# Performance work log

Measured on AMD Instinct MI355X. Metric: run time of the kernel, lower is better.

The kernel has to match this reference:

```python
import jax, jax.numpy as jnp
import numpy as np

D = 8        # num_decoders
N = 65536    # num_entries
LAT = 64     # latent_dim
HID = 128    # hidden_dim_dec
FEAT = 16    # feature_dim


def setup_inputs() -> dict:
    key = jax.random.key(0)
    ks = jax.random.split(key, 6)
    return {
        "weight": jax.random.normal(ks[0], (N, LAT), jnp.float32) * 2.0,
        "alpha_param": jax.random.normal(ks[1], (D, N), jnp.float32),  # alpha_std=1.0
        "div": jnp.ones((LAT,), jnp.float32),
        "scale0": jax.random.normal(ks[2], (D, LAT, HID), jnp.float32),  # ldec_std=1.0 normal init
        "shift0": jnp.zeros((D, 1, HID), jnp.float32),
        "scale1": jax.random.normal(ks[3], (D, HID, HID), jnp.float32),
        "shift1": jnp.zeros((D, 1, HID), jnp.float32),
        "scale2": jax.random.normal(ks[4], (D, HID, FEAT), jnp.float32),
        "shift2": jnp.zeros((D, 1, FEAT), jnp.float32),
    }


def _st_round(x):
    # StraightThrough: round in forward, identity gradient
    return x + jax.lax.stop_gradient(jnp.round(x) - x)


def _layer(x, alpha, scale, shift):
    # x: [N, I], alpha: [D, N], scale: [D, I, O], shift: [D, 1, O]
    out = jnp.einsum('ni,dio->dno', x, scale)           # per-decoder GEMMs [D,N,O]
    mix = jnp.einsum('dno,dn->no', out, alpha)          # alpha-weighted combine
    # second alpha-weighted sum over (mix + per-decoder shift), as in the torch code
    return jnp.einsum('dno,dn->no', mix[None, :, :] + shift, alpha)


def reference(weight, alpha_param, div, scale0, shift0, scale1, shift1, scale2, shift2):
    temperature = 1.0
    a = jax.nn.softmax(alpha_param / temperature, axis=0)       # [D, N]
    idx = jnp.argmax(a, axis=0)                                 # [N]
    onehot = jax.nn.one_hot(idx, a.shape[0], dtype=a.dtype).T   # [D, N]
    alpha = a + jax.lax.stop_gradient(onehot - a)               # straight-through one-hot

    x = _st_round(weight) / div                                 # [N, LAT]
    x = jax.nn.relu(_layer(x, alpha, scale0, shift0))           # [N, HID]
    x = jax.nn.relu(_layer(x, alpha, scale1, shift1))           # [N, HID]
    out = _layer(x, alpha, scale2, shift2)                      # [N, FEAT], final_activation='none'
    return out
```

## Files before the change

### kernel.cpp

```cpp
#include <hip/hip_runtime.h>

#define NN 65536
#define DD 8
#define LATD 64
#define HIDD 128
#define FEATD 16
#define BPD 96
#define SXS 72
#define SHS 136

typedef __attribute__((ext_vector_type(8))) short short8;
typedef __attribute__((ext_vector_type(4))) float f32x4;

static __device__ __forceinline__ unsigned short f2bf(float f) {
  union { float f; unsigned u; } v; v.f = f;
  unsigned r = v.u + 0x7FFFu + ((v.u >> 16) & 1u);
  return (unsigned short)(r >> 16);
}

__global__ __launch_bounds__(256) void k_bucket(const float* __restrict__ ap,
                                                int* __restrict__ cursor,
                                                unsigned short* __restrict__ perm) {
  __shared__ int bc[DD];
  __shared__ int bbase[DD];
  int t = threadIdx.x;
  if (t < DD) bc[t] = 0;
  __syncthreads();
  int n = blockIdx.x * 256 + t;
  float best = ap[n];
  int bd = 0;
#pragma unroll
  for (int d = 1; d < DD; ++d) {
    float v = ap[d * NN + n];
    if (v > best) { best = v; bd = d; }
  }
  int lr = atomicAdd(&bc[bd], 1);
  __syncthreads();
  if (t < DD) bbase[t] = atomicAdd(&cursor[t], bc[t]);
  __syncthreads();
  perm[bd * NN + bbase[bd] + lr] = (unsigned short)n;
}

__global__ __launch_bounds__(256, 3) void k_mlp(
    const float* __restrict__ weight, const float* __restrict__ divv,
    const float* __restrict__ s0, const float* __restrict__ sh0,
    const float* __restrict__ s1, const float* __restrict__ sh1,
    const float* __restrict__ s2, const float* __restrict__ sh2,
    const int* __restrict__ cursor, const unsigned short* __restrict__ perm,
    float* __restrict__ out) {
  __shared__ unsigned short sX[64 * SXS];
  __shared__ unsigned short sH1[64 * SHS];
  __shared__ unsigned short sH2[64 * SHS];
  __shared__ unsigned short sP[64];

  int d = blockIdx.x / BPD, bslot = blockIdx.x % BPD;
  int cnt = cursor[d];
  int t = threadIdx.x;
  int w = t >> 6, l = t & 63;
  int lrow = l & 15, kgrp = l >> 4;

  short8 b0[2][2];
  short8 b1[2][4];
  short8 b2[4];
  float sh0v[2], sh1v[2];
  const float* S0 = s0 + d * LATD * HIDD;
  const float* S1 = s1 + d * HIDD * HIDD;
  const float* S2 = s2 + d * HIDD * FEATD;
#pragma unroll
  for (int cb = 0; cb < 2; ++cb) {
    int n = (2 * w + cb) * 16 + lrow;
#pragma unroll
    for (int ks = 0; ks < 2; ++ks) {
      short8 v;
#pragma unroll
      for (int j = 0; j < 8; ++j)
        v[j] = (short)f2bf(S0[(ks * 32 + kgrp * 8 + j) * HIDD + n]);
      b0[cb][ks] = v;
    }
#pragma unroll
    for (int ks = 0; ks < 4; ++ks) {
      short8 v;
#pragma unroll
      for (int j = 0; j < 8; ++j)
        v[j] = (short)f2bf(S1[(ks * 32 + kgrp * 8 + j) * HIDD + n]);
      b1[cb][ks] = v;
    }
    sh0v[cb] = sh0[d * HIDD + n];
    sh1v[cb] = sh1[d * HIDD + n];
  }
#pragma unroll
  for (int ks = 0; ks < 4; ++ks) {
    short8 v;
#pragma unroll
    for (int j = 0; j < 8; ++j)
      v[j] = (short)f2bf(S2[(ks * 32 + kgrp * 8 + j) * FEATD + lrow]);
    b2[ks] = v;
  }
  float sh2v = sh2[d * FEATD + lrow];

  for (int tile = bslot; tile * 64 < cnt; tile += BPD) {
    int base = tile * 64;

    {
      int r = t >> 2, c = t & 3;
      int gp = base + r;
      unsigned short pe = 0;
      short8 lo = {0, 0, 0, 0, 0, 0, 0, 0}, hi = {0, 0, 0, 0, 0, 0, 0, 0};
      if (gp < cnt) {
        pe = perm[d * NN + gp];
        const float* wr = weight + (int)pe * LATD + c * 16;
        const float* dv = divv + c * 16;
#pragma unroll
        for (int q = 0; q < 2; ++q) {
          float4 f = *(const float4*)(wr + q * 4);
          float4 g = *(const float4*)(dv + q * 4);
          lo[q * 4 + 0] = (short)f2bf(rintf(f.x) / g.x);
          lo[q * 4 + 1] = (short)f2bf(rintf(f.y) / g.y);
          lo[q * 4 + 2] = (short)f2bf(rintf(f.z) / g.z);
          lo[q * 4 + 3] = (short)f2bf(rintf(f.w) / g.w);
        }
#pragma unroll
        for (int q = 0; q < 2; ++q) {
          float4 f = *(const float4*)(wr + 8 + q * 4);
          float4 g = *(const float4*)(dv + 8 + q * 4);
          hi[q * 4 + 0] = (short)f2bf(rintf(f.x) / g.x);
          hi[q * 4 + 1] = (short)f2bf(rintf(f.y) / g.y);
          hi[q * 4 + 2] = (short)f2bf(rintf(f.z) / g.z);
          hi[q * 4 + 3] = (short)f2bf(rintf(f.w) / g.w);
        }
      }
      if (c == 0) sP[r] = pe;
      *(short8*)&sX[r * SXS + c * 16] = lo;
      *(short8*)&sX[r * SXS + c * 16 + 8] = hi;
    }
    __syncthreads();

    int prow[4];
#pragma unroll
    for (int rr = 0; rr < 4; ++rr) prow[rr] = (int)sP[w * 16 + kgrp * 4 + rr];

#pragma unroll
    for (int rg = 0; rg < 4; ++rg) {
      short8 a0 = *(short8*)&sX[(rg * 16 + lrow) * SXS + kgrp * 8];
      short8 a1 = *(short8*)&sX[(rg * 16 + lrow) * SXS + 32 + kgrp * 8];
#pragma unroll
      for (int cb = 0; cb < 2; ++cb) {
        f32x4 acc = {sh0v[cb], sh0v[cb], sh0v[cb], sh0v[cb]};
        acc = __builtin_amdgcn_mfma_f32_16x16x32_bf16(a0, b0[cb][0], acc, 0, 0, 0);
        acc = __builtin_amdgcn_mfma_f32_16x16x32_bf16(a1, b0[cb][1], acc, 0, 0, 0);
#pragma unroll
        for (int rr = 0; rr < 4; ++rr)
          sH1[(rg * 16 + kgrp * 4 + rr) * SHS + (2 * w + cb) * 16 + lrow] =
              f2bf(fmaxf(acc[rr], 0.f));
      }
    }
    __syncthreads();

#pragma unroll
    for (int rg = 0; rg < 4; ++rg) {
      short8 h0 = *(short8*)&sH1[(rg * 16 + lrow) * SHS + kgrp * 8];
      short8 h1 = *(short8*)&sH1[(rg * 16 + lrow) * SHS + 32 + kgrp * 8];
      short8 h2 = *(short8*)&sH1[(rg * 16 + lrow) * SHS + 64 + kgrp * 8];
      short8 h3 = *(short8*)&sH1[(rg * 16 + lrow) * SHS + 96 + kgrp * 8];
#pragma unroll
      for (int cb = 0; cb < 2; ++cb) {
        f32x4 acc = {sh1v[cb], sh1v[cb], sh1v[cb], sh1v[cb]};
        acc = __builtin_amdgcn_mfma_f32_16x16x32_bf16(h0, b1[cb][0], acc, 0, 0, 0);
        acc = __builtin_amdgcn_mfma_f32_16x16x32_bf16(h1, b1[cb][1], acc, 0, 0, 0);
        acc = __builtin_amdgcn_mfma_f32_16x16x32_bf16(h2, b1[cb][2], acc, 0, 0, 0);
        acc = __builtin_amdgcn_mfma_f32_16x16x32_bf16(h3, b1[cb][3], acc, 0, 0, 0);
#pragma unroll
        for (int rr = 0; rr < 4; ++rr)
          sH2[(rg * 16 + kgrp * 4 + rr) * SHS + (2 * w + cb) * 16 + lrow] =
              f2bf(fmaxf(acc[rr], 0.f));
      }
    }
    __syncthreads();

    {
      short8 g0 = *(short8*)&sH2[(w * 16 + lrow) * SHS + kgrp * 8];
      short8 g1 = *(short8*)&sH2[(w * 16 + lrow) * SHS + 32 + kgrp * 8];
      short8 g2 = *(short8*)&sH2[(w * 16 + lrow) * SHS + 64 + kgrp * 8];
      short8 g3 = *(short8*)&sH2[(w * 16 + lrow) * SHS + 96 + kgrp * 8];
      f32x4 acc = {sh2v, sh2v, sh2v, sh2v};
      acc = __builtin_amdgcn_mfma_f32_16x16x32_bf16(g0, b2[0], acc, 0, 0, 0);
      acc = __builtin_amdgcn_mfma_f32_16x16x32_bf16(g1, b2[1], acc, 0, 0, 0);
      acc = __builtin_amdgcn_mfma_f32_16x16x32_bf16(g2, b2[2], acc, 0, 0, 0);
      acc = __builtin_amdgcn_mfma_f32_16x16x32_bf16(g3, b2[3], acc, 0, 0, 0);
#pragma unroll
      for (int rr = 0; rr < 4; ++rr) {
        int row = w * 16 + kgrp * 4 + rr;
        if (base + row < cnt) out[prow[rr] * FEATD + lrow] = acc[rr];
      }
    }
  }
}

extern "C" void kernel_launch(void* const* d_in, const int* in_sizes, int n_in,
                              void* d_out, int out_size, void* d_ws, size_t ws_size,
                              hipStream_t stream) {
  const float* weight      = (const float*)d_in[0];
  const float* alpha_param = (const float*)d_in[1];
  const float* divv        = (const float*)d_in[2];
  const float* scale0      = (const float*)d_in[3];
  const float* shift0      = (const float*)d_in[4];
  const float* scale1      = (const float*)d_in[5];
  const float* shift1      = (const float*)d_in[6];
  const float* scale2      = (const float*)d_in[7];
  const float* shift2      = (const float*)d_in[8];
  float* out = (float*)d_out;

  int* cursor = (int*)d_ws;
  unsigned short* perm = (unsigned short*)((int*)d_ws + 8);

  hipMemsetAsync(cursor, 0, DD * sizeof(int), stream);
  k_bucket<<<NN / 256, 256, 0, stream>>>(alpha_param, cursor, perm);
  k_mlp<<<DD * BPD, 256, 0, stream>>>(weight, divv,
                                      scale0, shift0, scale1, shift1,
                                      scale2, shift2,
                                      cursor, perm, out);
}
```

Baseline: 30.34 us.

## Pre-transpose decoder weights to bf16 in prep kernel; add MFMA setprio

The bucketing kernel now also converts the per-decoder scale matrices to bf16 in a transposed, K-contiguous layout in workspace. The MLP kernel can then fill its register B-fragments with vector loads instead of strided scalar fp32 loads and conversions in every block. MFMA sections are also wrapped in s_setprio to favour waves issuing matrix ops. This adds extra prep blocks, workspace traffic and a dependency between the two kernels.

```diff
diff --git a/kernel.cpp b/kernel.cpp
--- a/kernel.cpp
+++ b/kernel.cpp
@@ -11,6 +11,7 @@
 
 typedef __attribute__((ext_vector_type(8))) short short8;
 typedef __attribute__((ext_vector_type(4))) float f32x4;
+typedef __attribute__((ext_vector_type(8))) unsigned short ushort8;
 
 static __device__ __forceinline__ unsigned short f2bf(float f) {
   union { float f; unsigned u; } v; v.f = f;
@@ -18,34 +19,55 @@
   return (unsigned short)(r >> 16);
 }
 
-__global__ __launch_bounds__(256) void k_bucket(const float* __restrict__ ap,
-                                                int* __restrict__ cursor,
-                                                unsigned short* __restrict__ perm) {
-  __shared__ int bc[DD];
-  __shared__ int bbase[DD];
+__global__ __launch_bounds__(256) void k_prep(
+    const float* __restrict__ ap, int* __restrict__ cursor,
+    unsigned short* __restrict__ perm,
+    const float* __restrict__ s0, const float* __restrict__ s1,
+    const float* __restrict__ s2,
+    unsigned short* __restrict__ g0, unsigned short* __restrict__ g1,
+    unsigned short* __restrict__ g2) {
+  int bid = blockIdx.x;
   int t = threadIdx.x;
-  if (t < DD) bc[t] = 0;
-  __syncthreads();
-  int n = blockIdx.x * 256 + t;
-  float best = ap[n];
-  int bd = 0;
-#pragma unroll
-  for (int d = 1; d < DD; ++d) {
-    float v = ap[d * NN + n];
-    if (v > best) { best = v; bd = d; }
+  if (bid < 256) {
+    __shared__ int bc[DD];
+    __shared__ int bbase[DD];
+    if (t < DD) bc[t] = 0;
+    __syncthreads();
+    int n = bid * 256 + t;
+    float best = ap[n];
+    int bd = 0;
+#pragma unroll
+    for (int d = 1; d < DD; ++d) {
+      float v = ap[d * NN + n];
+      if (v > best) { best = v; bd = d; }
+    }
+    int lr = atomicAdd(&bc[bd], 1);
+    __syncthreads();
+    if (t < DD) bbase[t] = atomicAdd(&cursor[t], bc[t]);
+    __syncthreads();
+    perm[bd * NN + bbase[bd] + lr] = (unsigned short)n;
+  } else {
+    int o = (bid - 256) * 256 + t;
+    if (o < DD * HIDD * LATD) {
+      int d = o >> 13, rem = o & 8191, n = rem >> 6, k = rem & 63;
+      g0[o] = f2bf(s0[d * 8192 + k * 128 + n]);
+    }
+    if (o < DD * HIDD * HIDD) {
+      int d = o >> 14, rem = o & 16383, n = rem >> 7, k = rem & 127;
+      g1[o] = f2bf(s1[d * 16384 + k * 128 + n]);
+    }
+    if (o < DD * FEATD * HIDD) {
+      int d = o >> 11, rem = o & 2047, n = rem >> 7, k = rem & 127;
+      g2[o] = f2bf(s2[d * 2048 + k * 16 + n]);
+    }
   }
-  int lr = atomicAdd(&bc[bd], 1);
-  __syncthreads();
-  if (t < DD) bbase[t] = atomicAdd(&cursor[t], bc[t]);
-  __syncthreads();
-  perm[bd * NN + bbase[bd] + lr] = (unsigned short)n;
 }
 
 __global__ __launch_bounds__(256, 3) void k_mlp(
     const float* __restrict__ weight, const float* __restrict__ divv,
-    const float* __restrict__ s0, const float* __restrict__ sh0,
-    const float* __restrict__ s1, const float* __restrict__ sh1,
-    const float* __restrict__ s2, const float* __restrict__ sh2,
+    const unsigned short* __restrict__ g0, const float* __restrict__ sh0,
+    const unsigned short* __restrict__ g1, const float* __restrict__ sh1,
+    const unsigned short* __restrict__ g2, const float* __restrict__ sh2,
     const int* __restrict__ cursor, const unsigned short* __restrict__ perm,
     float* __restrict__ out) {
   __shared__ unsigned short sX[64 * SXS];
@@ -63,39 +85,24 @@
   short8 b1[2][4];
   short8 b2[4];
   float sh0v[2], sh1v[2];
-  const float* S0 = s0 + d * LATD * HIDD;
-  const float* S1 = s1 + d * HIDD * HIDD;
-  const float* S2 = s2 + d * HIDD * FEATD;
+  const unsigned short* G0 = g0 + d * (HIDD * LATD);
+  const unsigned short* G1 = g1 + d * (HIDD * HIDD);
+  const unsigned short* G2 = g2 + d * (FEATD * HIDD);
 #pragma unroll
   for (int cb = 0; cb < 2; ++cb) {
     int n = (2 * w + cb) * 16 + lrow;
 #pragma unroll
-    for (int ks = 0; ks < 2; ++ks) {
-      short8 v;
-#pragma unroll
-      for (int j = 0; j < 8; ++j)
-        v[j] = (short)f2bf(S0[(ks * 32 + kgrp * 8 + j) * HIDD + n]);
-      b0[cb][ks] = v;
-    }
-#pragma unroll
-    for (int ks = 0; ks < 4; ++ks) {
-      short8 v;
-#pragma unroll
-      for (int j = 0; j < 8; ++j)
-        v[j] = (short)f2bf(S1[(ks * 32 + kgrp * 8 + j) * HIDD + n]);
-      b1[cb][ks] = v;
-    }
+    for (int ks = 0; ks < 2; ++ks)
+      b0[cb][ks] = *(const short8*)&G0[n * LATD + ks * 32 + kgrp * 8];
+#pragma unroll
+    for (int ks = 0; ks < 4; ++ks)
+      b1[cb][ks] = *(const short8*)&G1[n * HIDD + ks * 32 + kgrp * 8];
     sh0v[cb] = sh0[d * HIDD + n];
     sh1v[cb] = sh1[d * HIDD + n];
   }
 #pragma unroll
-  for (int ks = 0; ks < 4; ++ks) {
-    short8 v;
-#pragma unroll
-    for (int j = 0; j < 8; ++j)
-      v[j] = (short)f2bf(S2[(ks * 32 + kgrp * 8 + j) * FEATD + lrow]);
-    b2[ks] = v;
-  }
+  for (int ks = 0; ks < 4; ++ks)
+    b2[ks] = *(const short8*)&G2[lrow * HIDD + ks * 32 + kgrp * 8];
   float sh2v = sh2[d * FEATD + lrow];
 
   for (int tile = bslot; tile * 64 < cnt; tile += BPD) {
@@ -143,6 +150,7 @@
     for (int rg = 0; rg < 4; ++rg) {
       short8 a0 = *(short8*)&sX[(rg * 16 + lrow) * SXS + kgrp * 8];
       short8 a1 = *(short8*)&sX[(rg * 16 + lrow) * SXS + 32 + kgrp * 8];
+      __builtin_amdgcn_s_setprio(1);
 #pragma unroll
       for (int cb = 0; cb < 2; ++cb) {
         f32x4 acc = {sh0v[cb], sh0v[cb], sh0v[cb], sh0v[cb]};
@@ -153,6 +161,7 @@
           sH1[(rg * 16 + kgrp * 4 + rr) * SHS + (2 * w + cb) * 16 + lrow] =
               f2bf(fmaxf(acc[rr], 0.f));
       }
+      __builtin_amdgcn_s_setprio(0);
     }
     __syncthreads();
 
@@ -162,6 +171,7 @@
       short8 h1 = *(short8*)&sH1[(rg * 16 + lrow) * SHS + 32 + kgrp * 8];
       short8 h2 = *(short8*)&sH1[(rg * 16 + lrow) * SHS + 64 + kgrp * 8];
       short8 h3 = *(short8*)&sH1[(rg * 16 + lrow) * SHS + 96 + kgrp * 8];
+      __builtin_amdgcn_s_setprio(1);
 #pragma unroll
       for (int cb = 0; cb < 2; ++cb) {
         f32x4 acc = {sh1v[cb], sh1v[cb], sh1v[cb], sh1v[cb]};
@@ -174,19 +184,22 @@
           sH2[(rg * 16 + kgrp * 4 + rr) * SHS + (2 * w + cb) * 16 + lrow] =
               f2bf(fmaxf(acc[rr], 0.f));
       }
+      __builtin_amdgcn_s_setprio(0);
     }
     __syncthreads();
 
     {
-      short8 g0 = *(short8*)&sH2[(w * 16 + lrow) * SHS + kgrp * 8];
-      short8 g1 = *(short8*)&sH2[(w * 16 + lrow) * SHS + 32 + kgrp * 8];
-      short8 g2 = *(short8*)&sH2[(w * 16 + lrow) * SHS + 64 + kgrp * 8];
-      short8 g3 = *(short8*)&sH2[(w * 16 + lrow) * SHS + 96 + kgrp * 8];
+      short8 q0 = *(short8*)&sH2[(w * 16 + lrow) * SHS + kgrp * 8];
+      short8 q1 = *(short8*)&sH2[(w * 16 + lrow) * SHS + 32 + kgrp * 8];
+      short8 q2 = *(short8*)&sH2[(w * 16 + lrow) * SHS + 64 + kgrp * 8];
+      short8 q3 = *(short8*)&sH2[(w * 16 + lrow) * SHS + 96 + kgrp * 8];
       f32x4 acc = {sh2v, sh2v, sh2v, sh2v};
-      acc = __builtin_amdgcn_mfma_f32_16x16x32_bf16(g0, b2[0], acc, 0, 0, 0);
-      acc = __builtin_amdgcn_mfma_f32_16x16x32_bf16(g1, b2[1], acc, 0, 0, 0);
-      acc = __builtin_amdgcn_mfma_f32_16x16x32_bf16(g2, b2[2], acc, 0, 0, 0);
-      acc = __builtin_amdgcn_mfma_f32_16x16x32_bf16(g3, b2[3], acc, 0, 0, 0);
+      __builtin_amdgcn_s_setprio(1);
+      acc = __builtin_amdgcn_mfma_f32_16x16x32_bf16(q0, b2[0], acc, 0, 0, 0);
+      acc = __builtin_amdgcn_mfma_f32_16x16x32_bf16(q1, b2[1], acc, 0, 0, 0);
+      acc = __builtin_amdgcn_mfma_f32_16x16x32_bf16(q2, b2[2], acc, 0, 0, 0);
+      acc = __builtin_amdgcn_mfma_f32_16x16x32_bf16(q3, b2[3], acc, 0, 0, 0);
+      __builtin_amdgcn_s_setprio(0);
 #pragma unroll
       for (int rr = 0; rr < 4; ++rr) {
         int row = w * 16 + kgrp * 4 + rr;
@@ -212,11 +225,14 @@
 
   int* cursor = (int*)d_ws;
   unsigned short* perm = (unsigned short*)((int*)d_ws + 8);
+  unsigned short* g0 = perm + DD * NN;
+  unsigned short* g1 = g0 + DD * HIDD * LATD;
+  unsigned short* g2 = g1 + DD * HIDD * HIDD;
 
   hipMemsetAsync(cursor, 0, DD * sizeof(int), stream);
-  k_bucket<<<NN / 256, 256, 0, stream>>>(alpha_param, cursor, perm);
+  k_prep<<<256 + 512, 256, 0, stream>>>(alpha_param, cursor, perm,
+                                        scale0, scale1, scale2, g0, g1, g2);
   k_mlp<<<DD * BPD, 256, 0, stream>>>(weight, divv,
-                                      scale0, shift0, scale1, shift1,
-                                      scale2, shift2,
+                                      g0, shift0, g1, shift1, g2, shift2,
                                       cursor, perm, out);
 }
```

New measurement: 31.45 us. +3.7%, slower.

## Replace global atomic bucketing with per-block histograms and in-kernel compaction

Applied to the files above, without the earlier changes.

The bucketing kernel now writes an 8-bit decoder index per entry plus a per-block histogram, which removes the global atomic cursor and the memset launch. Each MLP block scans the histogram prefix in shared memory, binary-searches for its tile, and rebuilds its 64-entry permutation by scanning packed index words with wave prefix sums. The aim is to drop the memset and the atomic contention and to get a deterministic ordering. In exchange, every tile now does extra scan work and adds a barrier. MFMA sections are also wrapped in s_setprio to raise wave priority during matrix math.

```diff
diff --git a/kernel.cpp b/kernel.cpp
--- a/kernel.cpp
+++ b/kernel.cpp
@@ -19,14 +19,13 @@
 }
 
 __global__ __launch_bounds__(256) void k_bucket(const float* __restrict__ ap,
-                                                int* __restrict__ cursor,
-                                                unsigned short* __restrict__ perm) {
+                                                unsigned* __restrict__ hist,
+                                                unsigned char* __restrict__ idx8) {
   __shared__ int bc[DD];
-  __shared__ int bbase[DD];
-  int t = threadIdx.x;
+  int t = threadIdx.x, bid = blockIdx.x;
   if (t < DD) bc[t] = 0;
   __syncthreads();
-  int n = blockIdx.x * 256 + t;
+  int n = bid * 256 + t;
   float best = ap[n];
   int bd = 0;
 #pragma unroll
@@ -34,11 +33,10 @@
     float v = ap[d * NN + n];
     if (v > best) { best = v; bd = d; }
   }
-  int lr = atomicAdd(&bc[bd], 1);
+  idx8[n] = (unsigned char)bd;
+  atomicAdd(&bc[bd], 1);
   __syncthreads();
-  if (t < DD) bbase[t] = atomicAdd(&cursor[t], bc[t]);
-  __syncthreads();
-  perm[bd * NN + bbase[bd] + lr] = (unsigned short)n;
+  if (t < DD) hist[t * 256 + bid] = (unsigned)bc[t];
 }
 
 __global__ __launch_bounds__(256, 3) void k_mlp(
@@ -46,113 +44,168 @@
     const float* __restrict__ s0, const float* __restrict__ sh0,
     const float* __restrict__ s1, const float* __restrict__ sh1,
     const float* __restrict__ s2, const float* __restrict__ sh2,
-    const int* __restrict__ cursor, const unsigned short* __restrict__ perm,
+    const unsigned* __restrict__ hist, const unsigned* __restrict__ idxw,
     float* __restrict__ out) {
   __shared__ unsigned short sX[64 * SXS];
   __shared__ unsigned short sH1[64 * SHS];
   __shared__ unsigned short sH2[64 * SHS];
-  __shared__ unsigned short sP[64];
-
-  int d = blockIdx.x / BPD, bslot = blockIdx.x % BPD;
-  int cnt = cursor[d];
-  int t = threadIdx.x;
+  __shared__ unsigned short sP16[64];
+  __shared__ unsigned sPfx[257];
+  __shared__ unsigned sWs[4];
+
+  int bid = blockIdx.x, t = threadIdx.x;
   int w = t >> 6, l = t & 63;
   int lrow = l & 15, kgrp = l >> 4;
-
-  short8 b0[2][2];
-  short8 b1[2][4];
-  short8 b2[4];
+  int d = bid / BPD, bslot = bid % BPD;
+
+  short8 b0f[2][2];
+  short8 b1f[2][4];
+  short8 b2f[4];
   float sh0v[2], sh1v[2];
-  const float* S0 = s0 + d * LATD * HIDD;
-  const float* S1 = s1 + d * HIDD * HIDD;
-  const float* S2 = s2 + d * HIDD * FEATD;
-#pragma unroll
-  for (int cb = 0; cb < 2; ++cb) {
-    int n = (2 * w + cb) * 16 + lrow;
-#pragma unroll
-    for (int ks = 0; ks < 2; ++ks) {
-      short8 v;
-#pragma unroll
-      for (int j = 0; j < 8; ++j)
-        v[j] = (short)f2bf(S0[(ks * 32 + kgrp * 8 + j) * HIDD + n]);
-      b0[cb][ks] = v;
+  {
+    const float* S0 = s0 + d * LATD * HIDD;
+    const float* S1 = s1 + d * HIDD * HIDD;
+    const float* S2 = s2 + d * HIDD * FEATD;
+#pragma unroll
+    for (int cb = 0; cb < 2; ++cb) {
+      int n2 = (2 * w + cb) * 16 + lrow;
+#pragma unroll
+      for (int ks = 0; ks < 2; ++ks) {
+        short8 v;
+#pragma unroll
+        for (int j = 0; j < 8; ++j)
+          v[j] = (short)f2bf(S0[(ks * 32 + kgrp * 8 + j) * HIDD + n2]);
+        b0f[cb][ks] = v;
+      }
+#pragma unroll
+      for (int ks = 0; ks < 4; ++ks) {
+        short8 v;
+#pragma unroll
+        for (int j = 0; j < 8; ++j)
+          v[j] = (short)f2bf(S1[(ks * 32 + kgrp * 8 + j) * HIDD + n2]);
+        b1f[cb][ks] = v;
+      }
+      sh0v[cb] = sh0[d * HIDD + n2];
+      sh1v[cb] = sh1[d * HIDD + n2];
     }
 #pragma unroll
     for (int ks = 0; ks < 4; ++ks) {
       short8 v;
 #pragma unroll
       for (int j = 0; j < 8; ++j)
-        v[j] = (short)f2bf(S1[(ks * 32 + kgrp * 8 + j) * HIDD + n]);
-      b1[cb][ks] = v;
-    }
-    sh0v[cb] = sh0[d * HIDD + n];
-    sh1v[cb] = sh1[d * HIDD + n];
-  }
-#pragma unroll
-  for (int ks = 0; ks < 4; ++ks) {
-    short8 v;
-#pragma unroll
-    for (int j = 0; j < 8; ++j)
-      v[j] = (short)f2bf(S2[(ks * 32 + kgrp * 8 + j) * FEATD + lrow]);
-    b2[ks] = v;
+        v[j] = (short)f2bf(S2[(ks * 32 + kgrp * 8 + j) * FEATD + lrow]);
+      b2f[ks] = v;
+    }
   }
   float sh2v = sh2[d * FEATD + lrow];
+
+  {
+    unsigned v = hist[d * 256 + t];
+    unsigned h = v;
+#pragma unroll
+    for (int off = 1; off < 64; off <<= 1) {
+      unsigned u = __shfl_up(v, off);
+      if (l >= off) v += u;
+    }
+    if (l == 63) sWs[w] = v;
+    __syncthreads();
+    unsigned woff = 0;
+#pragma unroll
+    for (int q = 0; q < 4; ++q)
+      if (q < w) woff += sWs[q];
+    if (t == 0) sPfx[0] = 0;
+    sPfx[t + 1] = v + woff;
+    (void)h;
+  }
+  __syncthreads();
+  int cnt = (int)sPfx[256];
 
   for (int tile = bslot; tile * 64 < cnt; tile += BPD) {
     int base = tile * 64;
+    int lim = min(base + 64, cnt);
+
+    {
+      int lo = 0, hi = 256;
+#pragma unroll
+      for (int it = 0; it < 8; ++it) {
+        int mid = (lo + hi) >> 1;
+        if ((int)sPfx[mid] <= base) lo = mid; else hi = mid;
+      }
+      for (int b = lo + w; b < 256 && (int)sPfx[b] < lim; b += 4) {
+        unsigned wd = idxw[b * 64 + l];
+        int m0 = ((wd) & 255) == d;
+        int m1 = ((wd >> 8) & 255) == d;
+        int m2 = ((wd >> 16) & 255) == d;
+        int m3 = ((wd >> 24)) == d;
+        int c4 = m0 + m1 + m2 + m3;
+        int sv = c4;
+#pragma unroll
+        for (int off = 1; off < 64; off <<= 1) {
+          int u = __shfl_up(sv, off);
+          if (l >= off) sv += u;
+        }
+        int rk = (int)sPfx[b] + sv - c4;
+        int nb = b * 256 + l * 4;
+        if (m0) { if (rk >= base && rk < lim) sP16[rk - base] = (unsigned short)(nb + 0); rk++; }
+        if (m1) { if (rk >= base && rk < lim) sP16[rk - base] = (unsigned short)(nb + 1); rk++; }
+        if (m2) { if (rk >= base && rk < lim) sP16[rk - base] = (unsigned short)(nb + 2); rk++; }
+        if (m3) { if (rk >= base && rk < lim) sP16[rk - base] = (unsigned short)(nb + 3); rk++; }
+      }
+    }
+    __syncthreads();
 
     {
       int r = t >> 2, c = t & 3;
       int gp = base + r;
-      unsigned short pe = 0;
-      short8 lo = {0, 0, 0, 0, 0, 0, 0, 0}, hi = {0, 0, 0, 0, 0, 0, 0, 0};
+      short8 lo8 = {0, 0, 0, 0, 0, 0, 0, 0}, hi8 = {0, 0, 0, 0, 0, 0, 0, 0};
       if (gp < cnt) {
-        pe = perm[d * NN + gp];
-        const float* wr = weight + (int)pe * LATD + c * 16;
+        int pe = (int)sP16[r];
+        const float* wr = weight + pe * LATD + c * 16;
         const float* dv = divv + c * 16;
 #pragma unroll
         for (int q = 0; q < 2; ++q) {
           float4 f = *(const float4*)(wr + q * 4);
           float4 g = *(const float4*)(dv + q * 4);
-          lo[q * 4 + 0] = (short)f2bf(rintf(f.x) / g.x);
-          lo[q * 4 + 1] = (short)f2bf(rintf(f.y) / g.y);
-          lo[q * 4 + 2] = (short)f2bf(rintf(f.z) / g.z);
-          lo[q * 4 + 3] = (short)f2bf(rintf(f.w) / g.w);
+          lo8[q * 4 + 0] = (short)f2bf(rintf(f.x) / g.x);
+          lo8[q * 4 + 1] = (short)f2bf(rintf(f.y) / g.y);
+          lo8[q * 4 + 2] = (short)f2bf(rintf(f.z) / g.z);
+          lo8[q * 4 + 3] = (short)f2bf(rintf(f.w) / g.w);
         }
 #pragma unroll
         for (int q = 0; q < 2; ++q) {
           float4 f = *(const float4*)(wr + 8 + q * 4);
           float4 g = *(const float4*)(dv + 8 + q * 4);
-          hi[q * 4 + 0] = (short)f2bf(rintf(f.x) / g.x);
-          hi[q * 4 + 1] = (short)f2bf(rintf(f.y) / g.y);
-          hi[q * 4 + 2] = (short)f2bf(rintf(f.z) / g.z);
-          hi[q * 4 + 3] = (short)f2bf(rintf(f.w) / g.w);
+          hi8[q * 4 + 0] = (short)f2bf(rintf(f.x) / g.x);
+          hi8[q * 4 + 1] = (short)f2bf(rintf(f.y) / g.y);
+          hi8[q * 4 + 2] = (short)f2bf(rintf(f.z) / g.z);
+          hi8[q * 4 + 3] = (short)f2bf(rintf(f.w) / g.w);
         }
       }
-      if (c == 0) sP[r] = pe;
-      *(short8*)&sX[r * SXS + c * 16] = lo;
-      *(short8*)&sX[r * SXS + c * 16 + 8] = hi;
+      *(short8*)&sX[r * SXS + c * 16] = lo8;
+      *(short8*)&sX[r * SXS + c * 16 + 8] = hi8;
     }
     __syncthreads();
 
     int prow[4];
 #pragma unroll
-    for (int rr = 0; rr < 4; ++rr) prow[rr] = (int)sP[w * 16 + kgrp * 4 + rr];
+    for (int rr = 0; rr < 4; ++rr) prow[rr] = (int)sP16[w * 16 + kgrp * 4 + rr];
 
 #pragma unroll
     for (int rg = 0; rg < 4; ++rg) {
       short8 a0 = *(short8*)&sX[(rg * 16 + lrow) * SXS + kgrp * 8];
       short8 a1 = *(short8*)&sX[(rg * 16 + lrow) * SXS + 32 + kgrp * 8];
+      __builtin_amdgcn_s_setprio(1);
 #pragma unroll
       for (int cb = 0; cb < 2; ++cb) {
         f32x4 acc = {sh0v[cb], sh0v[cb], sh0v[cb], sh0v[cb]};
-        acc = __builtin_amdgcn_mfma_f32_16x16x32_bf16(a0, b0[cb][0], acc, 0, 0, 0);
-        acc = __builtin_amdgcn_mfma_f32_16x16x32_bf16(a1, b0[cb][1], acc, 0, 0, 0);
+        acc = __builtin_amdgcn_mfma_f32_16x16x32_bf16(a0, b0f[cb][0], acc, 0, 0, 0);
+        acc = __builtin_amdgcn_mfma_f32_16x16x32_bf16(a1, b0f[cb][1], acc, 0, 0, 0);
 #pragma unroll
         for (int rr = 0; rr < 4; ++rr)
           sH1[(rg * 16 + kgrp * 4 + rr) * SHS + (2 * w + cb) * 16 + lrow] =
               f2bf(fmaxf(acc[rr], 0.f));
       }
+      __builtin_amdgcn_s_setprio(0);
     }
     __syncthreads();
 
@@ -162,37 +215,42 @@
       short8 h1 = *(short8*)&sH1[(rg * 16 + lrow) * SHS + 32 + kgrp * 8];
       short8 h2 = *(short8*)&sH1[(rg * 16 + lrow) * SHS + 64 + kgrp * 8];
       short8 h3 = *(short8*)&sH1[(rg * 16 + lrow) * SHS + 96 + kgrp * 8];
+      __builtin_amdgcn_s_setprio(1);
 #pragma unroll
       for (int cb = 0; cb < 2; ++cb) {
         f32x4 acc = {sh1v[cb], sh1v[cb], sh1v[cb], sh1v[cb]};
-        acc = __builtin_amdgcn_mfma_f32_16x16x32_bf16(h0, b1[cb][0], acc, 0, 0, 0);
-        acc = __builtin_amdgcn_mfma_f32_16x16x32_bf16(h1, b1[cb][1], acc, 0, 0, 0);
-        acc = __builtin_amdgcn_mfma_f32_16x16x32_bf16(h2, b1[cb][2], acc, 0, 0, 0);
-        acc = __builtin_amdgcn_mfma_f32_16x16x32_bf16(h3, b1[cb][3], acc, 0, 0, 0);
+        acc = __builtin_amdgcn_mfma_f32_16x16x32_bf16(h0, b1f[cb][0], acc, 0, 0, 0);
+        acc = __builtin_amdgcn_mfma_f32_16x16x32_bf16(h1, b1f[cb][1], acc, 0, 0, 0);
+        acc = __builtin_amdgcn_mfma_f32_16x16x32_bf16(h2, b1f[cb][2], acc, 0, 0, 0);
+        acc = __builtin_amdgcn_mfma_f32_16x16x32_bf16(h3, b1f[cb][3], acc, 0, 0, 0);
 #pragma unroll
         for (int rr = 0; rr < 4; ++rr)
           sH2[(rg * 16 + kgrp * 4 + rr) * SHS + (2 * w + cb) * 16 + lrow] =
               f2bf(fmaxf(acc[rr], 0.f));
       }
+      __builtin_amdgcn_s_setprio(0);
     }
     __syncthreads();
 
     {
-      short8 g0 = *(short8*)&sH2[(w * 16 + lrow) * SHS + kgrp * 8];
-      short8 g1 = *(short8*)&sH2[(w * 16 + lrow) * SHS + 32 + kgrp * 8];
-      short8 g2 = *(short8*)&sH2[(w * 16 + lrow) * SHS + 64 + kgrp * 8];
-      short8 g3 = *(short8*)&sH2[(w * 16 + lrow) * SHS + 96 + kgrp * 8];
+      short8 q0 = *(short8*)&sH2[(w * 16 + lrow) * SHS + kgrp * 8];
+      short8 q1 = *(short8*)&sH2[(w * 16 + lrow) * SHS + 32 + kgrp * 8];
+      short8 q2 = *(short8*)&sH2[(w * 16 + lrow) * SHS + 64 + kgrp * 8];
+      short8 q3 = *(short8*)&sH2[(w * 16 + lrow) * SHS + 96 + kgrp * 8];
       f32x4 acc = {sh2v, sh2v, sh2v, sh2v};
-      acc = __builtin_amdgcn_mfma_f32_16x16x32_bf16(g0, b2[0], acc, 0, 0, 0);
-      acc = __builtin_amdgcn_mfma_f32_16x16x32_bf16(g1, b2[1], acc, 0, 0, 0);
-      acc = __builtin_amdgcn_mfma_f32_16x16x32_bf16(g2, b2[2], acc, 0, 0, 0);
-      acc = __builtin_amdgcn_mfma_f32_16x16x32_bf16(g3, b2[3], acc, 0, 0, 0);
+      __builtin_amdgcn_s_setprio(1);
+      acc = __builtin_amdgcn_mfma_f32_16x16x32_bf16(q0, b2f[0], acc, 0, 0, 0);
+      acc = __builtin_amdgcn_mfma_f32_16x16x32_bf16(q1, b2f[1], acc, 0, 0, 0);
+      acc = __builtin_amdgcn_mfma_f32_16x16x32_bf16(q2, b2f[2], acc, 0, 0, 0);
+      acc = __builtin_amdgcn_mfma_f32_16x16x32_bf16(q3, b2f[3], acc, 0, 0, 0);
+      __builtin_amdgcn_s_setprio(0);
 #pragma unroll
       for (int rr = 0; rr < 4; ++rr) {
         int row = w * 16 + kgrp * 4 + rr;
         if (base + row < cnt) out[prow[rr] * FEATD + lrow] = acc[rr];
       }
     }
+    __syncthreads();
   }
 }
 
@@ -210,13 +268,12 @@
   const float* shift2      = (const float*)d_in[8];
   float* out = (float*)d_out;
 
-  int* cursor = (int*)d_ws;
-  unsigned short* perm = (unsigned short*)((int*)d_ws + 8);
-
-  hipMemsetAsync(cursor, 0, DD * sizeof(int), stream);
-  k_bucket<<<NN / 256, 256, 0, stream>>>(alpha_param, cursor, perm);
+  unsigned* hist = (unsigned*)d_ws;
+  unsigned char* idx8 = (unsigned char*)(hist + DD * 256);
+
+  k_bucket<<<NN / 256, 256, 0, stream>>>(alpha_param, hist, idx8);
   k_mlp<<<DD * BPD, 256, 0, stream>>>(weight, divv,
                                       scale0, shift0, scale1, shift1,
                                       scale2, shift2,
-                                      cursor, perm, out);
-}
+                                      hist, (const unsigned*)idx8, out);
+}
```

New measurement: 32.97 us. +8.7%, slower.
